# Optimization experiments

Hardware: AMD Instinct MI355X
Metric: run time of the kernel (lower is better)

Reference implementation:

```python
import jax, jax.numpy as jnp
import numpy as np

N, E, HID, H, D = 16000, 128000, 128, 8, 16
EPS = 1e-6
LN_EPS = 1e-5


def _ln(x, g, b):
    mu = x.mean(-1, keepdims=True)
    var = ((x - mu) ** 2).mean(-1, keepdims=True)
    return (x - mu) * jax.lax.rsqrt(var + LN_EPS) * g + b


def _phi(x):
    return jax.nn.elu(x) + 1.0


def setup_inputs() -> dict:
    key = jax.random.key(0)
    ks = jax.random.split(key, 16)
    w = lambda k, s: (jax.random.normal(k, s, jnp.float32) * 0.02)
    inp = {
        'x': jax.random.normal(ks[0], (N, HID), jnp.float32),
        'r': jax.random.normal(ks[1], (E, HID), jnp.float32),
        'edge_index': jax.random.randint(ks[2], (2, E), 0, N, jnp.int64),
        # layernorms
        'ln_x_g': jnp.ones((HID,)), 'ln_x_b': jnp.zeros((HID,)),
        'ln_r_g': jnp.ones((HID,)), 'ln_r_b': jnp.zeros((HID,)),
        'ln_post_g': jnp.ones((HID,)), 'ln_post_b': jnp.zeros((HID,)),
        'ln_ffpre_g': jnp.ones((HID,)), 'ln_ffpre_b': jnp.zeros((HID,)),
        'ln_ffpost_g': jnp.ones((HID,)), 'ln_ffpost_b': jnp.zeros((HID,)),
        # attention projections (stored [in, out]; y = x @ W)
        'Wq': w(ks[3], (HID, H * D)), 'Wk': w(ks[4], (HID, H * D)),
        'Wv': w(ks[5], (HID, H * D)),
        'Wkr': w(ks[6], (HID, H * D)), 'Wvr': w(ks[7], (HID, H * D)),
        'Wo': w(ks[8], (H * D, HID)),
        'Wg': w(ks[9], (2 * HID, HID)), 'bg': jnp.zeros((HID,)),
        'Ws': w(ks[10], (HID, HID)), 'bs': jnp.zeros((HID,)),
        # feed-forward
        'W1': w(ks[11], (HID, 4 * HID)), 'b1': jnp.zeros((4 * HID,)),
        'W2': w(ks[12], (4 * HID, HID)), 'b2': jnp.zeros((HID,)),
    }
    return inp


def reference(x, r, edge_index, ln_x_g, ln_x_b, ln_r_g, ln_r_b,
              ln_post_g, ln_post_b, ln_ffpre_g, ln_ffpre_b,
              ln_ffpost_g, ln_ffpost_b, Wq, Wk, Wv, Wkr, Wvr, Wo,
              Wg, bg, Ws, bs, W1, b1, W2, b2):
    n = x.shape[0]
    src, dst = edge_index[0], edge_index[1]
    xs = _ln(x, ln_x_g, ln_x_b)            # shared pre-norm (non-bipartite)
    rn = _ln(r, ln_r_g, ln_r_b)

    q = (xs @ Wq).reshape(n, H, D)
    k = (xs @ Wk).reshape(n, H, D)
    v = (xs @ Wv).reshape(n, H, D)
    k_e = k[src] + (rn @ Wkr).reshape(-1, H, D)   # [E,H,D]
    v_e = v[src] + (rn @ Wvr).reshape(-1, H, D)

    phi_q = _phi(q)                         # [N,H,D]
    phi_k = _phi(k_e)                       # [E,H,D]
    # per-edge outer product, scattered to destination nodes
    kv = phi_k[..., :, None] * v_e[..., None, :]          # [E,H,D,D]
    S = jax.ops.segment_sum(kv.reshape(-1, H * D * D), dst,
                            num_segments=n).reshape(n, H, D, D)
    Z = jax.ops.segment_sum(phi_k.reshape(-1, H * D), dst,
                            num_segments=n).reshape(n, H, D)

    num = jnp.einsum('nhd,nhdv->nhv', phi_q, S)
    den = jnp.maximum((phi_q * Z).sum(-1, keepdims=True), EPS)
    out = (num / den).reshape(n, H * D) @ Wo              # [N,HID]

    g = jax.nn.sigmoid(jnp.concatenate([out, xs], axis=-1) @ Wg + bg)
    attn = out + g * (xs @ Ws + bs - out)

    x_mid = x + _ln(attn, ln_post_g, ln_post_b)
    h = jax.nn.gelu(_ln(x_mid, ln_ffpre_g, ln_ffpre_b) @ W1 + b1,
                    approximate=False) @ W2 + b2
    return x_mid + _ln(h, ln_ffpost_g, ln_ffpost_b)
```

## Files before the change

kernel.cpp:

```cpp
#include <hip/hip_runtime.h>
#include <hip/hip_bf16.h>

#define NN 16000
#define NE 128000

typedef unsigned short u16;
typedef __attribute__((ext_vector_type(8))) short bf16x8;
typedef __attribute__((ext_vector_type(4))) float f32x4;

__device__ __forceinline__ float bf2f(u16 u) {
    unsigned int v = ((unsigned int)u) << 16;
    return __uint_as_float(v);
}
__device__ __forceinline__ u16 f2bf(float f) {
    unsigned int u = __float_as_uint(f);
    unsigned int r = u + 0x7FFF + ((u >> 16) & 1);
    return (u16)(r >> 16);
}
__device__ __forceinline__ float loadf(const void* p, size_t i, int bf) {
    return bf ? bf2f(((const u16*)p)[i]) : ((const float*)p)[i];
}

__device__ __forceinline__ int detect_bf(const u16* __restrict__ xw) {
    int lane = threadIdx.x & 63;
    int c = 0;
    #pragma unroll
    for (int k = 0; k < 16; ++k) {
        unsigned int w = xw[lane * 16 + k];
        int e = (int)((w >> 7) & 0xFF);
        c += (e >= 100 && e <= 140) ? 1 : 0;
    }
    for (int m = 1; m < 64; m <<= 1) c += __shfl_xor(c, m, 64);
    return c >= 850;
}

__device__ __forceinline__ int detect_e64(const int* __restrict__ ei) {
    int lane = threadIdx.x & 63;
    int a = 0;
    #pragma unroll
    for (int k = 0; k < 16; ++k) a |= ei[2 * (lane * 16 + k) + 1];
    for (int m = 1; m < 64; m <<= 1) a |= __shfl_xor(a, m, 64);
    return a == 0;
}

struct WDesc { const void* w; u16* wt; int K; int N; int off; int tile0; };
struct WTArgs { WDesc d[11]; };
__global__ __launch_bounds__(256) void pre1_kernel(const int* __restrict__ ei,
                                                   int* __restrict__ e32,
                                                   int* __restrict__ hist,
                                                   const u16* __restrict__ xw,
                                                   WTArgs args)
{
    int b = blockIdx.x;
    int tid = threadIdx.x;
    if (b < 250) {
        int e64 = detect_e64(ei);
        #pragma unroll
        for (int j = 0; j < 4; ++j) {
            int i = b * 1024 + j * 256 + tid;
            int v = e64 ? ei[2 * i] : ei[i];
            v = v < 0 ? 0 : (v >= NN ? NN - 1 : v);
            e32[i] = v;
            if (i >= NE) atomicAdd(&hist[v], 1);
        }
        return;
    }
    int bf = detect_bf(xw);
    int i = 0;
    while (i < 10 && b >= args.d[i + 1].tile0) ++i;
    WDesc de = args.d[i];
    int lt = b - de.tile0;
    int tn = de.N >> 5;
    int tk = lt / tn, tc = lt % tn;
    int n = tc * 32 + (tid & 31);
    int k = tk * 32 + ((tid >> 5) << 2);
    u16* dp = de.wt + (size_t)n * de.K + k;
    #pragma unroll
    for (int j = 0; j < 4; ++j)
        dp[j] = f2bf(loadf(de.w, (size_t)de.off + (size_t)(k + j) * de.N + n, bf));
}

__global__ __launch_bounds__(256) void scan_kernel(const int* __restrict__ hist,
                                                   int* __restrict__ offs,
                                                   int* __restrict__ cursor)
{
    __shared__ int wsum[4];
    __shared__ int carry_s;
    int tid = threadIdx.x, lane = tid & 63, w = tid >> 6;
    if (tid == 0) { carry_s = 0; offs[0] = 0; cursor[0] = 0; }
    __syncthreads();
    for (int c0 = 0; c0 < NN; c0 += 1024) {
        int i0 = c0 + tid * 4;
        int a0 = (i0 + 0 < NN) ? hist[i0 + 0] : 0;
        int a1 = (i0 + 1 < NN) ? hist[i0 + 1] : 0;
        int a2 = (i0 + 2 < NN) ? hist[i0 + 2] : 0;
        int a3 = (i0 + 3 < NN) ? hist[i0 + 3] : 0;
        int s_loc = a0 + a1 + a2 + a3;
        int x = s_loc;
        #pragma unroll
        for (int o = 1; o < 64; o <<= 1) {
            int y = __shfl_up(x, o, 64);
            if (lane >= o) x += y;
        }
        if (lane == 63) wsum[w] = x;
        __syncthreads();
        if (tid == 0) {
            int s = 0;
            #pragma unroll
            for (int j = 0; j < 4; ++j) { int t2 = wsum[j]; wsum[j] = s; s += t2; }
        }
        __syncthreads();
        int excl = x - s_loc + wsum[w] + carry_s;
        int p0 = excl + a0, p1 = p0 + a1, p2 = p1 + a2, p3 = p2 + a3;
        if (i0 + 0 < NN) { offs[i0 + 1] = p0; cursor[i0 + 1] = p0; }
        if (i0 + 1 < NN) { offs[i0 + 2] = p1; cursor[i0 + 2] = p1; }
        if (i0 + 2 < NN) { offs[i0 + 3] = p2; cursor[i0 + 3] = p2; }
        if (i0 + 3 < NN) { offs[i0 + 4] = p3; cursor[i0 + 4] = p3; }
        __syncthreads();
        if (tid == 255) carry_s = p3;
        __syncthreads();
    }
}

__global__ void scatter_kernel(const int* __restrict__ e32, int* __restrict__ cursor,
                               int* __restrict__ perm, int* __restrict__ ssrc,
                               int* __restrict__ sdst)
{
    int i = blockIdx.x * 256 + threadIdx.x;
    if (i >= NE) return;
    int d = e32[NE + i];
    int pos = atomicAdd(&cursor[d], 1);
    perm[pos] = i;
    ssrc[pos] = e32[i];
    sdst[pos] = d;
}

__global__ __launch_bounds__(256) void node_proj_kernel(
    const void* __restrict__ x,
    const void* __restrict__ lng, const void* __restrict__ lnb,
    const u16* __restrict__ Wall,
    const void* __restrict__ bs, const void* __restrict__ bg,
    u16* __restrict__ qkv, float* __restrict__ sbuf, float* __restrict__ gxs)
{
    const int bf = detect_bf((const u16*)x);
    __shared__ float sg[128], sb[128];
    int tid = threadIdx.x;
    if (tid < 128) { sg[tid] = loadf(lng, tid, bf); sb[tid] = loadf(lnb, tid, bf); }
    __syncthreads();
    int wave = tid >> 6, lane = tid & 63;
    int quad = lane >> 4, l15 = lane & 15;
    int m0 = blockIdx.x * 16;

    float vbuf[32];
    float s = 0.f, sq = 0.f;
    size_t rbase = (size_t)(m0 + l15) * 128;
    #pragma unroll
    for (int kc = 0; kc < 4; ++kc) {
        int cb = kc * 32 + quad * 8;
        if (bf) {
            ushort4 p0 = *(const ushort4*)((const u16*)x + rbase + cb);
            ushort4 p1 = *(const ushort4*)((const u16*)x + rbase + cb + 4);
            vbuf[kc*8+0]=bf2f(p0.x); vbuf[kc*8+1]=bf2f(p0.y); vbuf[kc*8+2]=bf2f(p0.z); vbuf[kc*8+3]=bf2f(p0.w);
            vbuf[kc*8+4]=bf2f(p1.x); vbuf[kc*8+5]=bf2f(p1.y); vbuf[kc*8+6]=bf2f(p1.z); vbuf[kc*8+7]=bf2f(p1.w);
        } else {
            float4 p0 = *(const float4*)((const float*)x + rbase + cb);
            float4 p1 = *(const float4*)((const float*)x + rbase + cb + 4);
            vbuf[kc*8+0]=p0.x; vbuf[kc*8+1]=p0.y; vbuf[kc*8+2]=p0.z; vbuf[kc*8+3]=p0.w;
            vbuf[kc*8+4]=p1.x; vbuf[kc*8+5]=p1.y; vbuf[kc*8+6]=p1.z; vbuf[kc*8+7]=p1.w;
        }
        #pragma unroll
        for (int j = 0; j < 8; ++j) { s += vbuf[kc*8+j]; sq += vbuf[kc*8+j]*vbuf[kc*8+j]; }
    }
    s += __shfl_xor(s, 16, 64); sq += __shfl_xor(sq, 16, 64);
    s += __shfl_xor(s, 32, 64); sq += __shfl_xor(sq, 32, 64);
    float mu = s * (1.0f / 128.0f);
    float var = sq * (1.0f / 128.0f) - mu * mu;
    float rsx = rsqrtf(var + 1e-5f);
    bf16x8 afr[4];
    #pragma unroll
    for (int kc = 0; kc < 4; ++kc) {
        bf16x8 a;
        #pragma unroll
        for (int j = 0; j < 8; ++j) {
            int col = kc * 32 + quad * 8 + j;
            a[j] = (short)f2bf((vbuf[kc*8+j] - mu) * rsx * sg[col] + sb[col]);
        }
        afr[kc] = a;
    }

    f32x4 acc[10] = {};
    #pragma unroll
    for (int kc = 0; kc < 4; ++kc)
        #pragma unroll
        for (int tt = 0; tt < 10; ++tt) {
            int t = wave * 10 + tt;
            bf16x8 b = *(const bf16x8*)(Wall + (size_t)(t * 16 + l15) * 128 + kc * 32 + quad * 8);
            acc[tt] = __builtin_amdgcn_mfma_f32_16x16x32_bf16(afr[kc], b, acc[tt], 0, 0, 0);
        }
    #pragma unroll
    for (int tt = 0; tt < 10; ++tt) {
        int ct = (wave * 10 + tt) * 16 + l15;
        #pragma unroll
        for (int rg = 0; rg < 4; ++rg) {
            int row = m0 + quad * 4 + rg;
            float v = acc[tt][rg];
            if (ct < 384) {
                if (ct < 128) v = (v > 0.0f) ? v + 1.0f : expf(v);
                qkv[(size_t)row * 384 + ct] = f2bf(v);
            } else if (ct < 512) {
                int cs = ct - 384;
                sbuf[(size_t)row * 128 + cs] = v + loadf(bs, cs, bf);
            } else {
                int cg = ct - 512;
                gxs[(size_t)row * 128 + cg] = v + loadf(bg, cg, bf);
            }
        }
    }
}

__global__ __launch_bounds__(256) void edge_proj_kernel(
    const void* __restrict__ r, const void* __restrict__ x,
    const void* __restrict__ lng, const void* __restrict__ lnb,
    const u16* __restrict__ Wkrt, const u16* __restrict__ Wvrt,
    const int* __restrict__ perm, const int* __restrict__ ssrc,
    const int* __restrict__ sdst,
    const u16* __restrict__ qkv,
    float* __restrict__ p_arr, u16* __restrict__ ve_s)
{
    const int bf = detect_bf((const u16*)x);
    __shared__ float sg[128], sb[128];
    int tid = threadIdx.x;
    if (tid < 128) { sg[tid] = loadf(lng, tid, bf); sb[tid] = loadf(lnb, tid, bf); }
    __syncthreads();
    int wave = tid >> 6, lane = tid & 63;
    int quad = lane >> 4, l15 = lane & 15;
    int e0 = blockIdx.x * 32 + (wave >> 1) * 16;
    int c0 = (wave & 1) * 64;

    int rrow = perm[e0 + l15];
    float vbuf[32];
    float s = 0.f, sq = 0.f;
    size_t rbase = (size_t)rrow * 128;
    #pragma unroll
    for (int kc = 0; kc < 4; ++kc) {
        int cb = kc * 32 + quad * 8;
        if (bf) {
            ushort4 p0 = *(const ushort4*)((const u16*)r + rbase + cb);
            ushort4 p1 = *(const ushort4*)((const u16*)r + rbase + cb + 4);
            vbuf[kc*8+0]=bf2f(p0.x); vbuf[kc*8+1]=bf2f(p0.y); vbuf[kc*8+2]=bf2f(p0.z); vbuf[kc*8+3]=bf2f(p0.w);
            vbuf[kc*8+4]=bf2f(p1.x); vbuf[kc*8+5]=bf2f(p1.y); vbuf[kc*8+6]=bf2f(p1.z); vbuf[kc*8+7]=bf2f(p1.w);
        } else {
            float4 p0 = *(const float4*)((const float*)r + rbase + cb);
            float4 p1 = *(const float4*)((const float*)r + rbase + cb + 4);
            vbuf[kc*8+0]=p0.x; vbuf[kc*8+1]=p0.y; vbuf[kc*8+2]=p0.z; vbuf[kc*8+3]=p0.w;
            vbuf[kc*8+4]=p1.x; vbuf[kc*8+5]=p1.y; vbuf[kc*8+6]=p1.z; vbuf[kc*8+7]=p1.w;
        }
        #pragma unroll
        for (int j = 0; j < 8; ++j) { s += vbuf[kc*8+j]; sq += vbuf[kc*8+j]*vbuf[kc*8+j]; }
    }
    s += __shfl_xor(s, 16, 64); sq += __shfl_xor(sq, 16, 64);
    s += __shfl_xor(s, 32, 64); sq += __shfl_xor(sq, 32, 64);
    float mu = s * (1.0f / 128.0f);
    float var = sq * (1.0f / 128.0f) - mu * mu;
    float rsx = rsqrtf(var + 1e-5f);
    bf16x8 afr[4];
    #pragma unroll
    for (int kc = 0; kc < 4; ++kc) {
        bf16x8 a;
        #pragma unroll
        for (int j = 0; j < 8; ++j) {
            int col = kc * 32 + quad * 8 + j;
            a[j] = (short)f2bf((vbuf[kc*8+j] - mu) * rsx * sg[col] + sb[col]);
        }
        afr[kc] = a;
    }

    f32x4 acck[4] = {};
    f32x4 accv[4] = {};
    #pragma unroll
    for (int kc = 0; kc < 4; ++kc) {
        int k0 = kc * 32;
        #pragma unroll
        for (int t = 0; t < 4; ++t) {
            bf16x8 bk = *(const bf16x8*)(Wkrt + (size_t)(c0 + t*16 + l15) * 128 + k0 + quad * 8);
            bf16x8 bv = *(const bf16x8*)(Wvrt + (size_t)(c0 + t*16 + l15) * 128 + k0 + quad * 8);
            acck[t] = __builtin_amdgcn_mfma_f32_16x16x32_bf16(afr[kc], bk, acck[t], 0, 0, 0);
            accv[t] = __builtin_amdgcn_mfma_f32_16x16x32_bf16(afr[kc], bv, accv[t], 0, 0, 0);
        }
    }

    int se[4], de[4];
    #pragma unroll
    for (int rg = 0; rg < 4; ++rg) {
        int e = e0 + quad * 4 + rg;
        se[rg] = ssrc[e]; de[rg] = sdst[e];
    }
    #pragma unroll
    for (int t = 0; t < 4; ++t) {
        int col = c0 + t * 16 + l15;
        float p_[4];
        #pragma unroll
        for (int rg = 0; rg < 4; ++rg) {
            float kv = acck[t][rg] + bf2f(qkv[(size_t)se[rg] * 384 + 128 + col]);
            kv = (kv > 0.0f) ? kv + 1.0f : expf(kv);
            float pm = kv * bf2f(qkv[(size_t)de[rg] * 384 + col]);
            pm += __shfl_xor(pm, 1, 64);
            pm += __shfl_xor(pm, 2, 64);
            pm += __shfl_xor(pm, 4, 64);
            pm += __shfl_xor(pm, 8, 64);
            p_[rg] = pm;
        }
        if (l15 == 0) {
            #pragma unroll
            for (int rg = 0; rg < 4; ++rg)
                p_arr[(size_t)(e0 + quad * 4 + rg) * 8 + (c0 >> 4) + t] = p_[rg];
        }
        #pragma unroll
        for (int rg = 0; rg < 4; ++rg) {
            float vv = accv[t][rg] + bf2f(qkv[(size_t)se[rg] * 384 + 256 + col]);
            ve_s[(size_t)(e0 + quad * 4 + rg) * 128 + col] = f2bf(vv);
        }
    }
}

__global__ __launch_bounds__(256) void node_acc_kernel(
    const float* __restrict__ p_arr, const u16* __restrict__ ve_s,
    const int* __restrict__ offs, float* __restrict__ att)
{
    int n = blockIdx.x * 4 + (threadIdx.x >> 6);
    int lane = threadIdx.x & 63;
    int beg = offs[n], end = offs[n + 1];
    int h = lane >> 3;
    float na0 = 0.f, na1 = 0.f, da = 0.f;
    float nb0 = 0.f, nb1 = 0.f, db = 0.f;
    int e = beg;
    for (; e + 1 < end; e += 2) {
        float pa = p_arr[(size_t)e * 8 + h];
        float pb = p_arr[(size_t)(e + 1) * 8 + h];
        ushort2 va = *(const ushort2*)&ve_s[(size_t)e * 128 + 2 * lane];
        ushort2 vb = *(const ushort2*)&ve_s[(size_t)(e + 1) * 128 + 2 * lane];
        na0 += pa * bf2f(va.x); na1 += pa * bf2f(va.y); da += pa;
        nb0 += pb * bf2f(vb.x); nb1 += pb * bf2f(vb.y); db += pb;
    }
    if (e < end) {
        float pa = p_arr[(size_t)e * 8 + h];
        ushort2 va = *(const ushort2*)&ve_s[(size_t)e * 128 + 2 * lane];
        na0 += pa * bf2f(va.x); na1 += pa * bf2f(va.y); da += pa;
    }
    float inv = 1.0f / fmaxf(da + db, 1e-6f);
    att[(size_t)n * 128 + 2 * lane]     = (na0 + nb0) * inv;
    att[(size_t)n * 128 + 2 * lane + 1] = (na1 + nb1) * inv;
}

__global__ __launch_bounds__(256) void gate_mega_kernel(
    const float* __restrict__ att,
    const u16* __restrict__ Wo_t, const u16* __restrict__ Wg1_t,
    const float* __restrict__ gxs, const float* __restrict__ sbuf,
    const void* __restrict__ x,
    const void* __restrict__ g_po, const void* __restrict__ b_po,
    const void* __restrict__ g_fp, const void* __restrict__ b_fp,
    float* __restrict__ xmid, u16* __restrict__ ffp)
{
    const int bf = detect_bf((const u16*)x);
    __shared__ float lds[4][16][132];
    __shared__ float sgpo[128], sbpo[128], sgfp[128], sbfp[128];
    int tid = threadIdx.x;
    if (tid < 128) {
        sgpo[tid] = loadf(g_po, tid, bf);
        sbpo[tid] = loadf(b_po, tid, bf);
        sgfp[tid] = loadf(g_fp, tid, bf);
        sbfp[tid] = loadf(b_fp, tid, bf);
    }
    __syncthreads();
    int wave = tid >> 6, lane = tid & 63;
    int quad = lane >> 4, l15 = lane & 15;
    int m0 = blockIdx.x * 64 + wave * 16;

    bf16x8 ahi[4], alo[4];
    #pragma unroll
    for (int kc = 0; kc < 4; ++kc) {
        const float* ap = att + (size_t)(m0 + l15) * 128 + kc * 32 + quad * 8;
        float4 v0 = *(const float4*)ap;
        float4 v1 = *(const float4*)(ap + 4);
        float vv[8] = {v0.x, v0.y, v0.z, v0.w, v1.x, v1.y, v1.z, v1.w};
        bf16x8 h, l;
        #pragma unroll
        for (int j = 0; j < 8; ++j) {
            u16 hb = f2bf(vv[j]);
            h[j] = (short)hb;
            l[j] = (short)f2bf(vv[j] - bf2f(hb));
        }
        ahi[kc] = h; alo[kc] = l;
    }
    f32x4 acco[8] = {};
    #pragma unroll
    for (int kc = 0; kc < 4; ++kc)
        #pragma unroll
        for (int t = 0; t < 8; ++t) {
            bf16x8 b = *(const bf16x8*)(Wo_t + (size_t)(t*16 + l15) * 128 + kc*32 + quad*8);
            acco[t] = __builtin_amdgcn_mfma_f32_16x16x32_bf16(ahi[kc], b, acco[t], 0, 0, 0);
            acco[t] = __builtin_amdgcn_mfma_f32_16x16x32_bf16(alo[kc], b, acco[t], 0, 0, 0);
        }
    #pragma unroll
    for (int t = 0; t < 8; ++t)
        #pragma unroll
        for (int rg = 0; rg < 4; ++rg)
            lds[wave][quad*4+rg][t*16+l15] = acco[t][rg];
    __syncthreads();
    bf16x8 afo[4];
    #pragma unroll
    for (int kc = 0; kc < 4; ++kc) {
        bf16x8 a;
        #pragma unroll
        for (int j = 0; j < 8; ++j)
            a[j] = (short)f2bf(lds[wave][l15][kc*32 + quad*8 + j]);
        afo[kc] = a;
    }
    f32x4 accg[8] = {};
    #pragma unroll
    for (int kc = 0; kc < 4; ++kc)
        #pragma unroll
        for (int t = 0; t < 8; ++t) {
            bf16x8 b = *(const bf16x8*)(Wg1_t + (size_t)(t*16 + l15) * 128 + kc*32 + quad*8);
            accg[t] = __builtin_amdgcn_mfma_f32_16x16x32_bf16(afo[kc], b, accg[t], 0, 0, 0);
        }
    float attn[8][4];
    float sv[4] = {0,0,0,0}, sqv[4] = {0,0,0,0};
    #pragma unroll
    for (int t = 0; t < 8; ++t) {
        int col = t * 16 + l15;
        #pragma unroll
        for (int rg = 0; rg < 4; ++rg) {
            int row = m0 + quad * 4 + rg;
            float gp = accg[t][rg] + gxs[(size_t)row * 128 + col];
            float gg = 1.0f / (1.0f + expf(-gp));
            float o = acco[t][rg];
            float a = o + gg * (sbuf[(size_t)row * 128 + col] - o);
            attn[t][rg] = a; sv[rg] += a; sqv[rg] += a * a;
        }
    }
    #pragma unroll
    for (int rg = 0; rg < 4; ++rg)
        for (int m = 1; m < 16; m <<= 1) {
            sv[rg] += __shfl_xor(sv[rg], m, 64);
            sqv[rg] += __shfl_xor(sqv[rg], m, 64);
        }
    float mu[4], rs[4];
    #pragma unroll
    for (int rg = 0; rg < 4; ++rg) {
        mu[rg] = sv[rg] * (1.0f / 128.0f);
        float var = sqv[rg] * (1.0f / 128.0f) - mu[rg] * mu[rg];
        rs[rg] = rsqrtf(var + 1e-5f);
    }
    float s2[4] = {0,0,0,0}, sq2[4] = {0,0,0,0};
    #pragma unroll
    for (int t = 0; t < 8; ++t) {
        int col = t * 16 + l15;
        #pragma unroll
        for (int rg = 0; rg < 4; ++rg) {
            int row = m0 + quad * 4 + rg;
            float xm = loadf(x, (size_t)row * 128 + col, bf)
                     + (attn[t][rg] - mu[rg]) * rs[rg] * sgpo[col] + sbpo[col];
            attn[t][rg] = xm;
            xmid[(size_t)row * 128 + col] = xm;
            s2[rg] += xm; sq2[rg] += xm * xm;
        }
    }
    #pragma unroll
    for (int rg = 0; rg < 4; ++rg)
        for (int m = 1; m < 16; m <<= 1) {
            s2[rg] += __shfl_xor(s2[rg], m, 64);
            sq2[rg] += __shfl_xor(sq2[rg], m, 64);
        }
    #pragma unroll
    for (int rg = 0; rg < 4; ++rg) {
        float mu2 = s2[rg] * (1.0f / 128.0f);
        float var2 = sq2[rg] * (1.0f / 128.0f) - mu2 * mu2;
        float rs2 = rsqrtf(var2 + 1e-5f);
        #pragma unroll
        for (int t = 0; t < 8; ++t) {
            int col = t * 16 + l15;
            int row = m0 + quad * 4 + rg;
            ffp[(size_t)row * 128 + col] =
                f2bf((attn[t][rg] - mu2) * rs2 * sgfp[col] + sbfp[col]);
        }
    }
}

__global__ __launch_bounds__(256) void ff_mega_kernel(
    const u16* __restrict__ ffp, const u16* __restrict__ W1_t, const void* __restrict__ b1,
    const u16* __restrict__ W2_t, const void* __restrict__ b2,
    const float* __restrict__ xmid, const void* __restrict__ x,
    const void* __restrict__ g_fo, const void* __restrict__ b_fo,
    void* __restrict__ outp)
{
    const int bf = detect_bf((const u16*)x);
    __shared__ __align__(16) u16 h1l[16][520];
    __shared__ float psum[4][16], psq[4][16];
    int tid = threadIdx.x;
    int wave = tid >> 6, lane = tid & 63;
    int quad = lane >> 4, l15 = lane & 15;
    int m0 = blockIdx.x * 16;

    bf16x8 afr[4];
    const u16* ap = ffp + (size_t)(m0 + l15) * 128 + quad * 8;
    #pragma unroll
    for (int kc = 0; kc < 4; ++kc) afr[kc] = *(const bf16x8*)(ap + kc * 32);

    f32x4 acc1[8] = {};
    #pragma unroll
    for (int kc = 0; kc < 4; ++kc)
        #pragma unroll
        for (int tt = 0; tt < 8; ++tt) {
            int t = wave * 8 + tt;
            bf16x8 b = *(const bf16x8*)(W1_t + (size_t)(t*16 + l15) * 128 + kc*32 + quad*8);
            acc1[tt] = __builtin_amdgcn_mfma_f32_16x16x32_bf16(afr[kc], b, acc1[tt], 0, 0, 0);
        }
    #pragma unroll
    for (int tt = 0; tt < 8; ++tt) {
        int col = (wave * 8 + tt) * 16 + l15;
        float bv = loadf(b1, col, bf);
        #pragma unroll
        for (int rg = 0; rg < 4; ++rg) {
            float v = acc1[tt][rg] + bv;
            v = 0.5f * v * (1.0f + erff(v * 0.70710678118f));
            h1l[quad * 4 + rg][col] = f2bf(v);
        }
    }
    __syncthreads();
    f32x4 acc2[2] = {};
    #pragma unroll
    for (int kc = 0; kc < 16; ++kc) {
        bf16x8 a = *(const bf16x8*)&h1l[l15][kc * 32 + quad * 8];
        #pragma unroll
        for (int tt = 0; tt < 2; ++tt) {
            int t = wave * 2 + tt;
            bf16x8 b = *(const bf16x8*)(W2_t + (size_t)(t*16 + l15) * 512 + kc*32 + quad*8);
            acc2[tt] = __builtin_amdgcn_mfma_f32_16x16x32_bf16(a, b, acc2[tt], 0, 0, 0);
        }
    }
    float h2v[2][4];
    float sv[4] = {0,0,0,0}, sqv[4] = {0,0,0,0};
    #pragma unroll
    for (int tt = 0; tt < 2; ++tt) {
        int col = (wave * 2 + tt) * 16 + l15;
        float bv = loadf(b2, col, bf);
        #pragma unroll
        for (int rg = 0; rg < 4; ++rg) {
            float v = acc2[tt][rg] + bv;
            h2v[tt][rg] = v; sv[rg] += v; sqv[rg] += v * v;
        }
    }
    #pragma unroll
    for (int rg = 0; rg < 4; ++rg)
        for (int m = 1; m < 16; m <<= 1) {
            sv[rg] += __shfl_xor(sv[rg], m, 64);
            sqv[rg] += __shfl_xor(sqv[rg], m, 64);
        }
    if (l15 == 0) {
        #pragma unroll
        for (int rg = 0; rg < 4; ++rg) {
            psum[wave][quad * 4 + rg] = sv[rg];
            psq[wave][quad * 4 + rg]  = sqv[rg];
        }
    }
    __syncthreads();
    #pragma unroll
    for (int rg = 0; rg < 4; ++rg) {
        int rl = quad * 4 + rg;
        float ts = psum[0][rl] + psum[1][rl] + psum[2][rl] + psum[3][rl];
        float tq = psq[0][rl]  + psq[1][rl]  + psq[2][rl]  + psq[3][rl];
        float mu = ts * (1.0f / 128.0f);
        float var = tq * (1.0f / 128.0f) - mu * mu;
        float rs = rsqrtf(var + 1e-5f);
        int row = m0 + rl;
        #pragma unroll
        for (int tt = 0; tt < 2; ++tt) {
            int col = (wave * 2 + tt) * 16 + l15;
            float y = xmid[(size_t)row * 128 + col]
                    + (h2v[tt][rg] - mu) * rs * loadf(g_fo, col, bf) + loadf(b_fo, col, bf);
            if (bf) ((u16*)outp)[(size_t)row * 128 + col] = f2bf(y);
            else    ((float*)outp)[(size_t)row * 128 + col] = y;
        }
    }
}

extern "C" void kernel_launch(void* const* d_in, const int* in_sizes, int n_in,
                              void* d_out, int out_size, void* d_ws, size_t ws_size,
                              hipStream_t stream)
{
    const int N = NN, E = NE;
    const void* x       = d_in[0];
    const void* r       = d_in[1];
    const int*  ei      = (const int*)d_in[2];
    const void* ln_x_g  = d_in[3];
    const void* ln_x_b  = d_in[4];
    const void* ln_r_g  = d_in[5];
    const void* ln_r_b  = d_in[6];
    const void* ln_po_g = d_in[7];
    const void* ln_po_b = d_in[8];
    const void* ln_fp_g = d_in[9];
    const void* ln_fp_b = d_in[10];
    const void* ln_fo_g = d_in[11];
    const void* ln_fo_b = d_in[12];
    const void* Wq      = d_in[13];
    const void* Wk      = d_in[14];
    const void* Wv      = d_in[15];
    const void* Wkr     = d_in[16];
    const void* Wvr     = d_in[17];
    const void* Wo      = d_in[18];
    const void* Wg      = d_in[19];
    const void* bg      = d_in[20];
    const void* Ws      = d_in[21];
    const void* bs      = d_in[22];
    const void* W1      = d_in[23];
    const void* b1      = d_in[24];
    const void* W2      = d_in[25];
    const void* b2      = d_in[26];

    float* ws = (float*)d_ws;
    size_t off = 0;
    auto alloc = [&](size_t n) { float* p = ws + off; off += n; return p; };
    const size_t U = (size_t)N * 64;
    u16*   qkv_bf = (u16*)alloc(3 * U);
    float* att    = alloc((size_t)N * 128);
    float* sbuf   = alloc((size_t)N * 128);
    float* gxs    = alloc((size_t)N * 128);
    float* xmid   = alloc((size_t)N * 128);
    u16*   ffp_bf = (u16*)alloc(U);
    u16*   ve_s   = (u16*)alloc((size_t)E * 64);
    float* p_arr  = alloc((size_t)E * 8);
    int*   e32    = (int*)alloc((size_t)2 * E);
    int*   perm   = (int*)alloc(E);
    int*   ssrc   = (int*)alloc(E);
    int*   sdst   = (int*)alloc(E);
    int*   hist   = (int*)alloc(NN);
    int*   offs   = (int*)alloc(NN + 1);
    int*   cursor = (int*)alloc(NN + 1);
    u16*   wt     = (u16*)alloc(139264);

    u16* Wall_t = wt;
    u16* Wkr_t  = wt + 81920;
    u16* Wvr_t  = wt + 98304;
    u16* Wo_t   = wt + 114688;
    u16* Wg1_t  = wt + 131072;
    u16* W1_t   = wt + 147456;
    u16* W2_t   = wt + 212992;

    hipMemsetAsync(hist, 0, NN * sizeof(int), stream);

    WTArgs wa;
    int t0 = 250;
    auto setw = [&](int i, const void* w, u16* wtp, int K, int Ncol, int eoff) {
        wa.d[i] = WDesc{w, wtp, K, Ncol, eoff, t0};
        t0 += (K / 32) * (Ncol / 32);
    };
    setw(0, Wq,  wt,           128, 128, 0);
    setw(1, Wk,  wt + 16384,   128, 128, 0);
    setw(2, Wv,  wt + 32768,   128, 128, 0);
    setw(3, Ws,  wt + 49152,   128, 128, 0);
    setw(4, Wg,  wt + 65536,   128, 128, 16384);
    setw(5, Wkr, Wkr_t,        128, 128, 0);
    setw(6, Wvr, Wvr_t,        128, 128, 0);
    setw(7, Wo,  Wo_t,         128, 128, 0);
    setw(8, Wg,  Wg1_t,        128, 128, 0);
    setw(9, W1,  W1_t,         128, 512, 0);
    setw(10, W2, W2_t,         512, 128, 0);
    pre1_kernel<<<t0, 256, 0, stream>>>(ei, e32, hist, (const u16*)x, wa);

    scan_kernel<<<1, 256, 0, stream>>>(hist, offs, cursor);
    scatter_kernel<<<(E + 255) / 256, 256, 0, stream>>>(e32, cursor, perm, ssrc, sdst);

    node_proj_kernel<<<N / 16, 256, 0, stream>>>(x, ln_x_g, ln_x_b, Wall_t,
                                                 bs, bg, qkv_bf, sbuf, gxs);

    edge_proj_kernel<<<E / 32, 256, 0, stream>>>(r, x, ln_r_g, ln_r_b, Wkr_t, Wvr_t,
                                                 perm, ssrc, sdst, qkv_bf, p_arr, ve_s);

    node_acc_kernel<<<N / 4, 256, 0, stream>>>(p_arr, ve_s, offs, att);

    gate_mega_kernel<<<N / 64, 256, 0, stream>>>(att, Wo_t, Wg1_t, gxs, sbuf,
                                                 x, ln_po_g, ln_po_b, ln_fp_g, ln_fp_b,
                                                 xmid, ffp_bf);

    ff_mega_kernel<<<N / 16, 256, 0, stream>>>(ffp_bf, W1_t, b1, W2_t, b2,
                                               xmid, x, ln_fo_g, ln_fo_b, d_out);
}
```

Measured before the change: 395.6 us.

## Fuse edge aggregation into edge projection via segmented atomic accumulation

The per-node accumulation kernel is removed. The edge projection kernel now does a segmented reduction in LDS over each wave's 16 dst-sorted edges and atomically adds the numerator and denominator into node buffers. Normalisation by the denominator moves into the gate kernel. This drops the per-edge p_arr and ve_s round trip through global memory and one launch, at the cost of float atomics, extra LDS, a wider per-wave tile with more registers, and a larger memset.

```diff
diff --git a/kernel.cpp b/kernel.cpp
--- a/kernel.cpp
+++ b/kernel.cpp
@@ -225,19 +225,20 @@
     const int* __restrict__ perm, const int* __restrict__ ssrc,
     const int* __restrict__ sdst,
     const u16* __restrict__ qkv,
-    float* __restrict__ p_arr, u16* __restrict__ ve_s)
+    float* __restrict__ num, float* __restrict__ den)
 {
     const int bf = detect_bf((const u16*)x);
     __shared__ float sg[128], sb[128];
+    __shared__ float pv[4][16][132];
+    __shared__ float pden[4][16][8];
     int tid = threadIdx.x;
     if (tid < 128) { sg[tid] = loadf(lng, tid, bf); sb[tid] = loadf(lnb, tid, bf); }
     __syncthreads();
     int wave = tid >> 6, lane = tid & 63;
     int quad = lane >> 4, l15 = lane & 15;
-    int e0 = blockIdx.x * 32 + (wave >> 1) * 16;
-    int c0 = (wave & 1) * 64;
-
-    int rrow = perm[e0 + l15];
+    int ew0 = blockIdx.x * 64 + wave * 16;
+
+    int rrow = perm[ew0 + l15];
     float vbuf[32];
     float s = 0.f, sq = 0.f;
     size_t rbase = (size_t)rrow * 128;
@@ -275,15 +276,15 @@
         afr[kc] = a;
     }
 
-    f32x4 acck[4] = {};
-    f32x4 accv[4] = {};
+    f32x4 acck[8] = {};
+    f32x4 accv[8] = {};
     #pragma unroll
     for (int kc = 0; kc < 4; ++kc) {
         int k0 = kc * 32;
         #pragma unroll
-        for (int t = 0; t < 4; ++t) {
-            bf16x8 bk = *(const bf16x8*)(Wkrt + (size_t)(c0 + t*16 + l15) * 128 + k0 + quad * 8);
-            bf16x8 bv = *(const bf16x8*)(Wvrt + (size_t)(c0 + t*16 + l15) * 128 + k0 + quad * 8);
+        for (int t = 0; t < 8; ++t) {
+            bf16x8 bk = *(const bf16x8*)(Wkrt + (size_t)(t*16 + l15) * 128 + k0 + quad * 8);
+            bf16x8 bv = *(const bf16x8*)(Wvrt + (size_t)(t*16 + l15) * 128 + k0 + quad * 8);
             acck[t] = __builtin_amdgcn_mfma_f32_16x16x32_bf16(afr[kc], bk, acck[t], 0, 0, 0);
             accv[t] = __builtin_amdgcn_mfma_f32_16x16x32_bf16(afr[kc], bv, accv[t], 0, 0, 0);
         }
@@ -292,13 +293,12 @@
     int se[4], de[4];
     #pragma unroll
     for (int rg = 0; rg < 4; ++rg) {
-        int e = e0 + quad * 4 + rg;
+        int e = ew0 + quad * 4 + rg;
         se[rg] = ssrc[e]; de[rg] = sdst[e];
     }
     #pragma unroll
-    for (int t = 0; t < 4; ++t) {
-        int col = c0 + t * 16 + l15;
-        float p_[4];
+    for (int t = 0; t < 8; ++t) {
+        int col = t * 16 + l15;
         #pragma unroll
         for (int rg = 0; rg < 4; ++rg) {
             float kv = acck[t][rg] + bf2f(qkv[(size_t)se[rg] * 384 + 128 + col]);
@@ -308,52 +308,33 @@
             pm += __shfl_xor(pm, 2, 64);
             pm += __shfl_xor(pm, 4, 64);
             pm += __shfl_xor(pm, 8, 64);
-            p_[rg] = pm;
-        }
-        if (l15 == 0) {
-            #pragma unroll
-            for (int rg = 0; rg < 4; ++rg)
-                p_arr[(size_t)(e0 + quad * 4 + rg) * 8 + (c0 >> 4) + t] = p_[rg];
-        }
-        #pragma unroll
-        for (int rg = 0; rg < 4; ++rg) {
             float vv = accv[t][rg] + bf2f(qkv[(size_t)se[rg] * 384 + 256 + col]);
-            ve_s[(size_t)(e0 + quad * 4 + rg) * 128 + col] = f2bf(vv);
-        }
-    }
-}
-
-__global__ __launch_bounds__(256) void node_acc_kernel(
-    const float* __restrict__ p_arr, const u16* __restrict__ ve_s,
-    const int* __restrict__ offs, float* __restrict__ att)
-{
-    int n = blockIdx.x * 4 + (threadIdx.x >> 6);
-    int lane = threadIdx.x & 63;
-    int beg = offs[n], end = offs[n + 1];
-    int h = lane >> 3;
-    float na0 = 0.f, na1 = 0.f, da = 0.f;
-    float nb0 = 0.f, nb1 = 0.f, db = 0.f;
-    int e = beg;
-    for (; e + 1 < end; e += 2) {
-        float pa = p_arr[(size_t)e * 8 + h];
-        float pb = p_arr[(size_t)(e + 1) * 8 + h];
-        ushort2 va = *(const ushort2*)&ve_s[(size_t)e * 128 + 2 * lane];
-        ushort2 vb = *(const ushort2*)&ve_s[(size_t)(e + 1) * 128 + 2 * lane];
-        na0 += pa * bf2f(va.x); na1 += pa * bf2f(va.y); da += pa;
-        nb0 += pb * bf2f(vb.x); nb1 += pb * bf2f(vb.y); db += pb;
-    }
-    if (e < end) {
-        float pa = p_arr[(size_t)e * 8 + h];
-        ushort2 va = *(const ushort2*)&ve_s[(size_t)e * 128 + 2 * lane];
-        na0 += pa * bf2f(va.x); na1 += pa * bf2f(va.y); da += pa;
-    }
-    float inv = 1.0f / fmaxf(da + db, 1e-6f);
-    att[(size_t)n * 128 + 2 * lane]     = (na0 + nb0) * inv;
-    att[(size_t)n * 128 + 2 * lane + 1] = (na1 + nb1) * inv;
+            pv[wave][quad * 4 + rg][col] = pm * vv;
+            if (l15 == 0) pden[wave][quad * 4 + rg][t] = pm;
+        }
+    }
+    float rs0 = 0.f, rs1 = 0.f, rden = 0.f;
+    int prev = sdst[ew0];
+    for (int row = 0; row < 16; ++row) {
+        int d = sdst[ew0 + row];
+        if (d != prev) {
+            atomicAdd(&num[(size_t)prev * 128 + 2 * lane], rs0);
+            atomicAdd(&num[(size_t)prev * 128 + 2 * lane + 1], rs1);
+            if (lane < 8) atomicAdd(&den[prev * 8 + lane], rden);
+            rs0 = rs1 = rden = 0.f;
+            prev = d;
+        }
+        float2 v2 = *(const float2*)&pv[wave][row][2 * lane];
+        rs0 += v2.x; rs1 += v2.y;
+        if (lane < 8) rden += pden[wave][row][lane];
+    }
+    atomicAdd(&num[(size_t)prev * 128 + 2 * lane], rs0);
+    atomicAdd(&num[(size_t)prev * 128 + 2 * lane + 1], rs1);
+    if (lane < 8) atomicAdd(&den[prev * 8 + lane], rden);
 }
 
 __global__ __launch_bounds__(256) void gate_mega_kernel(
-    const float* __restrict__ att,
+    const float* __restrict__ num, const float* __restrict__ den,
     const u16* __restrict__ Wo_t, const u16* __restrict__ Wg1_t,
     const float* __restrict__ gxs, const float* __restrict__ sbuf,
     const void* __restrict__ x,
@@ -379,16 +360,19 @@
     bf16x8 ahi[4], alo[4];
     #pragma unroll
     for (int kc = 0; kc < 4; ++kc) {
-        const float* ap = att + (size_t)(m0 + l15) * 128 + kc * 32 + quad * 8;
-        float4 v0 = *(const float4*)ap;
-        float4 v1 = *(const float4*)(ap + 4);
+        int cb = kc * 32 + quad * 8;
+        const float* np = num + (size_t)(m0 + l15) * 128 + cb;
+        float inv = 1.0f / fmaxf(den[(m0 + l15) * 8 + (cb >> 4)], 1e-6f);
+        float4 v0 = *(const float4*)np;
+        float4 v1 = *(const float4*)(np + 4);
         float vv[8] = {v0.x, v0.y, v0.z, v0.w, v1.x, v1.y, v1.z, v1.w};
         bf16x8 h, l;
         #pragma unroll
         for (int j = 0; j < 8; ++j) {
-            u16 hb = f2bf(vv[j]);
+            float a = vv[j] * inv;
+            u16 hb = f2bf(a);
             h[j] = (short)hb;
-            l[j] = (short)f2bf(vv[j] - bf2f(hb));
+            l[j] = (short)f2bf(a - bf2f(hb));
         }
         ahi[kc] = h; alo[kc] = l;
     }
@@ -611,8 +595,8 @@
     const void* Wo      = d_in[18];
     const void* Wg      = d_in[19];
     const void* bg      = d_in[20];
+    const void* bs      = d_in[22];
     const void* Ws      = d_in[21];
-    const void* bs      = d_in[22];
     const void* W1      = d_in[23];
     const void* b1      = d_in[24];
     const void* W2      = d_in[25];
@@ -622,19 +606,18 @@
     size_t off = 0;
     auto alloc = [&](size_t n) { float* p = ws + off; off += n; return p; };
     const size_t U = (size_t)N * 64;
+    float* num    = alloc((size_t)N * 128);
+    float* den    = alloc((size_t)N * 8);
+    int*   hist   = (int*)alloc(NN);
     u16*   qkv_bf = (u16*)alloc(3 * U);
-    float* att    = alloc((size_t)N * 128);
     float* sbuf   = alloc((size_t)N * 128);
     float* gxs    = alloc((size_t)N * 128);
     float* xmid   = alloc((size_t)N * 128);
     u16*   ffp_bf = (u16*)alloc(U);
-    u16*   ve_s   = (u16*)alloc((size_t)E * 64);
-    float* p_arr  = alloc((size_t)E * 8);
     int*   e32    = (int*)alloc((size_t)2 * E);
     int*   perm   = (int*)alloc(E);
     int*   ssrc   = (int*)alloc(E);
     int*   sdst   = (int*)alloc(E);
-    int*   hist   = (int*)alloc(NN);
     int*   offs   = (int*)alloc(NN + 1);
     int*   cursor = (int*)alloc(NN + 1);
     u16*   wt     = (u16*)alloc(139264);
@@ -647,7 +630,7 @@
     u16* W1_t   = wt + 147456;
     u16* W2_t   = wt + 212992;
 
-    hipMemsetAsync(hist, 0, NN * sizeof(int), stream);
+    hipMemsetAsync(num, 0, ((size_t)N * 128 + (size_t)N * 8 + NN) * sizeof(float), stream);
 
     WTArgs wa;
     int t0 = 250;
@@ -674,12 +657,10 @@
     node_proj_kernel<<<N / 16, 256, 0, stream>>>(x, ln_x_g, ln_x_b, Wall_t,
                                                  bs, bg, qkv_bf, sbuf, gxs);
 
-    edge_proj_kernel<<<E / 32, 256, 0, stream>>>(r, x, ln_r_g, ln_r_b, Wkr_t, Wvr_t,
-                                                 perm, ssrc, sdst, qkv_bf, p_arr, ve_s);
-
-    node_acc_kernel<<<N / 4, 256, 0, stream>>>(p_arr, ve_s, offs, att);
-
-    gate_mega_kernel<<<N / 64, 256, 0, stream>>>(att, Wo_t, Wg1_t, gxs, sbuf,
+    edge_proj_kernel<<<E / 64, 256, 0, stream>>>(r, x, ln_r_g, ln_r_b, Wkr_t, Wvr_t,
+                                                 perm, ssrc, sdst, qkv_bf, num, den);
+
+    gate_mega_kernel<<<N / 64, 256, 0, stream>>>(num, den, Wo_t, Wg1_t, gxs, sbuf,
                                                  x, ln_po_g, ln_po_b, ln_fp_g, ln_fp_b,
                                                  xmid, ffp_bf);
 
```

New measurement: 429.2 us. +8.5%, slower.
